# Optimization experiments

Hardware: AMD Instinct MI355X
Metric: run time of the kernel (lower is better)

Reference implementation:

```python
import jax, jax.numpy as jnp
import numpy as np

EMBED_DIM = 512
NUM_HEADS = 16
WIN = (8, 8)
N_TOK = WIN[0] * WIN[1]           # 64 tokens per window
HEAD_DIM = EMBED_DIM // NUM_HEADS  # 32
SCALE = HEAD_DIM ** -0.5
B_WIN = 1024                       # batch * num_windows
NUM_WINDOWS = 256                  # windows per image -> batch images = 4


def _relative_bias_index(window_size):
    wh, ww = window_size
    coords = np.stack(np.meshgrid(np.arange(wh), np.arange(ww), indexing='ij'))  # (2, wh, ww)
    flat = coords.reshape(2, -1)                                   # (2, N)
    rel = (flat[:, :, None] - flat[:, None, :]).transpose(1, 2, 0)  # (N, N, 2)
    rel[:, :, 0] += wh - 1
    rel[:, :, 1] += ww - 1
    rel[:, :, 0] *= 2 * ww - 1
    return rel.sum(-1)  # (N, N) int


def setup_inputs() -> dict:
    key = jax.random.key(0)
    ks = jax.random.split(key, 6)
    x = jax.random.normal(ks[0], (B_WIN, N_TOK, EMBED_DIM), dtype=jnp.float32)
    attention_mask = jax.random.normal(ks[1], (NUM_WINDOWS, N_TOK, N_TOK), dtype=jnp.float32)
    qkv_w = jax.random.normal(ks[2], (EMBED_DIM, 3 * EMBED_DIM), dtype=jnp.float32) * 0.02
    qkv_b = jnp.zeros((3 * EMBED_DIM,), dtype=jnp.float32)
    proj_w = jax.random.normal(ks[3], (EMBED_DIM, EMBED_DIM), dtype=jnp.float32) * 0.02
    proj_b = jnp.zeros((EMBED_DIM,), dtype=jnp.float32)
    n_bias = (2 * WIN[0] - 1) * (2 * WIN[1] - 1)  # 225
    bias_table = jax.random.normal(ks[4], (n_bias, NUM_HEADS), dtype=jnp.float32) * 0.02
    rel_index = jnp.asarray(_relative_bias_index(WIN), dtype=jnp.int32)  # (N, N)
    return {"x": x, "attention_mask": attention_mask, "qkv_w": qkv_w, "qkv_b": qkv_b,
            "proj_w": proj_w, "proj_b": proj_b, "bias_table": bias_table, "rel_index": rel_index}


def reference(x, attention_mask, qkv_w, qkv_b, proj_w, proj_b, bias_table, rel_index):
    B, N, C = x.shape
    nw = attention_mask.shape[0]
    bimg = B // nw
    qkv = x @ qkv_w + qkv_b                              # (B, N, 3C)
    # original rearrange 'b n (h d c) -> d b n h c' groups last dim as (heads, 3, head_dim)
    qkv = qkv.reshape(B, N, NUM_HEADS, 3, HEAD_DIM)
    q, k, v = qkv[..., 0, :], qkv[..., 1, :], qkv[..., 2, :]  # each (B, N, H, hd)
    attn = jnp.einsum('bqhd,bkhd->bhqk', q, k) * SCALE        # (B, H, N, N)
    bias = bias_table[rel_index].transpose(2, 0, 1)           # (H, N, N)
    attn = attn + bias[None]
    attn = attn.reshape(bimg, nw, NUM_HEADS, N, N) + attention_mask[None, :, None]
    attn = jax.nn.softmax(attn, axis=-1).reshape(B, NUM_HEADS, N, N)
    out = jnp.einsum('bhqk,bkhd->bqhd', attn, v).reshape(B, N, C)
    return out @ proj_w + proj_b
```

## Files before the change

### kernel.cpp

```cpp
#include <hip/hip_runtime.h>
#include <hip/hip_bf16.h>


typedef unsigned short u16;
typedef __bf16 bx8 __attribute__((ext_vector_type(8)));
typedef float f4_t __attribute__((ext_vector_type(4)));

#define QKV_ELEMS 33554432ull
#define SCALE 0.17677669529663687f

static __device__ __forceinline__ u16 f2b(float f) {
    return __builtin_bit_cast(u16, (__bf16)f);
}

typedef const unsigned int __attribute__((address_space(1)))* gas_t;
typedef unsigned int __attribute__((address_space(3)))* las_t;
static __device__ __forceinline__ void glds16(const void* g, void* l) {
    __builtin_amdgcn_global_load_lds((gas_t)g, (las_t)l, 16, 0, 0);
}

__global__ void cvt_k(const float* __restrict__ X, u16* __restrict__ Xb) {
    size_t i = ((size_t)blockIdx.x * 256 + threadIdx.x) * 8;
    float4 v0 = *(const float4*)(X + i);
    float4 v1 = *(const float4*)(X + i + 4);
    ushort4 p0, p1;
    p0.x = f2b(v0.x); p0.y = f2b(v0.y); p0.z = f2b(v0.z); p0.w = f2b(v0.w);
    p1.x = f2b(v1.x); p1.y = f2b(v1.y); p1.z = f2b(v1.z); p1.w = f2b(v1.w);
    *(ushort4*)(Xb + i) = p0;
    *(ushort4*)(Xb + i + 4) = p1;
}

__global__ void wt_k(const float* __restrict__ W, u16* __restrict__ Wt,
                     int K, int N) {
    int idx = blockIdx.x * 256 + threadIdx.x;
    if (idx >= N * K) return;
    int n = idx / K, k = idx - n * K;
    Wt[idx] = f2b(W[(size_t)k * N + n]);
}

__global__ void bias_k(const float* __restrict__ bias_table,
                       const int* __restrict__ rel_index,
                       float* __restrict__ bias_full) {
    int idx = blockIdx.x * 256 + threadIdx.x;
    int h = idx >> 12, rc = idx & 4095;
    bias_full[idx] = bias_table[rel_index[rc] * 16 + h];
}

template <int MODE>
__global__ __launch_bounds__(256) void gemm_k(
    const u16* __restrict__ A, const u16* __restrict__ Bt,
    const float* __restrict__ bias, void* __restrict__ Out, int K) {
    const int tid  = threadIdx.x;
    const int wave = tid >> 6, lane = tid & 63;
    const int quad = lane >> 4, l16 = lane & 15;
    const int wm = wave >> 1, wn = wave & 1;
    const int m0 = blockIdx.y * 128, n0 = blockIdx.x * 128;
    const int N = gridDim.x * 128;

    __shared__ alignas(16) u16 a_s[128 * 32];
    __shared__ alignas(16) u16 b_s[128 * 32];

    const int lr = lane >> 2, lc = (lane & 3) * 8;
    const int w16 = wave * 16;

    f4_t acc[4][4];
#pragma unroll
    for (int i = 0; i < 4; ++i)
#pragma unroll
        for (int j = 0; j < 4; ++j) acc[i][j] = (f4_t){0.f, 0.f, 0.f, 0.f};

    for (int kt = 0; kt < K; kt += 32) {
        const u16* Ab = A + (size_t)m0 * K + kt;
        const u16* Bb = Bt + (size_t)n0 * K + kt;
        glds16(Ab + (size_t)(w16 + lr) * K + lc,      &a_s[w16 * 32]);
        glds16(Ab + (size_t)(w16 + 64 + lr) * K + lc, &a_s[(w16 + 64) * 32]);
        glds16(Bb + (size_t)(w16 + lr) * K + lc,      &b_s[w16 * 32]);
        glds16(Bb + (size_t)(w16 + 64 + lr) * K + lc, &b_s[(w16 + 64) * 32]);
        __syncthreads();

        bx8 af[4], bfr[4];
#pragma unroll
        for (int mt = 0; mt < 4; ++mt)
            af[mt] = *(const bx8*)&a_s[(wm * 64 + mt * 16 + l16) * 32 + quad * 8];
#pragma unroll
        for (int nt = 0; nt < 4; ++nt)
            bfr[nt] = *(const bx8*)&b_s[(wn * 64 + nt * 16 + l16) * 32 + quad * 8];
#pragma unroll
        for (int mt = 0; mt < 4; ++mt)
#pragma unroll
            for (int nt = 0; nt < 4; ++nt)
                acc[mt][nt] = __builtin_amdgcn_mfma_f32_16x16x32_bf16(
                    af[mt], bfr[nt], acc[mt][nt], 0, 0, 0);
        __syncthreads();
    }

    if (MODE == 0) {
        u16* qkv = (u16*)Out;
#pragma unroll
        for (int mt = 0; mt < 4; ++mt)
#pragma unroll
            for (int nt = 0; nt < 4; ++nt)
#pragma unroll
                for (int i = 0; i < 4; ++i) {
                    int r = m0 + wm * 64 + mt * 16 + quad * 4 + i;
                    int c = n0 + wn * 64 + nt * 16 + l16;
                    float v = acc[mt][nt][i] + bias[c];
                    int w = r >> 6, tok = r & 63;
                    int h = c / 96, rr = c - h * 96;
                    int which = rr >> 5, dd = rr & 31;
                    qkv[(size_t)which * QKV_ELEMS +
                        ((size_t)((w * 16 + h) * 64 + tok)) * 32 + dd] = f2b(v);
                }
    } else {
        float* Of = (float*)Out;
#pragma unroll
        for (int mt = 0; mt < 4; ++mt)
#pragma unroll
            for (int nt = 0; nt < 4; ++nt)
#pragma unroll
                for (int i = 0; i < 4; ++i) {
                    int r = m0 + wm * 64 + mt * 16 + quad * 4 + i;
                    int c = n0 + wn * 64 + nt * 16 + l16;
                    Of[(size_t)r * N + c] = acc[mt][nt][i] + bias[c];
                }
    }
}

__global__ __launch_bounds__(256) void attn_k(
    const u16* __restrict__ qkv, const float* __restrict__ mask,
    const float* __restrict__ biasf, u16* __restrict__ attn_out) {
    const int bx = blockIdx.x;
    const int w = bx >> 4, h = bx & 15;
    const int wmk = w & 255;
    const int tid = threadIdx.x;
    const int wave = tid >> 6, lane = tid & 63;
    const int quad = lane >> 4, l16 = lane & 15;

    __shared__ alignas(16) u16 q_s[64 * 40];
    __shared__ alignas(16) u16 k_s[64 * 40];
    __shared__ alignas(16) u16 vT[32 * 72];
    __shared__ float s_s[64 * 68];
    __shared__ alignas(16) u16 p_s[64 * 72];

    const size_t base = (size_t)((w << 4) + h) * 2048;
    {
        int tok = tid >> 2, d0 = (tid & 3) * 8;
        uint4 qv = *(const uint4*)(qkv + base + tid * 8);
        *(uint4*)&q_s[tok * 40 + d0] = qv;
        uint4 kv = *(const uint4*)(qkv + QKV_ELEMS + base + tid * 8);
        *(uint4*)&k_s[tok * 40 + d0] = kv;
        uint4 vv = *(const uint4*)(qkv + 2 * QKV_ELEMS + base + tid * 8);
        const u16* pv = (const u16*)&vv;
#pragma unroll
        for (int j = 0; j < 8; ++j) vT[(d0 + j) * 72 + tok] = pv[j];
    }
    __syncthreads();

    {
        bx8 a = *(const bx8*)&q_s[(wave * 16 + l16) * 40 + quad * 8];
#pragma unroll
        for (int nt = 0; nt < 4; ++nt) {
            bx8 b = *(const bx8*)&k_s[(nt * 16 + l16) * 40 + quad * 8];
            f4_t acc = (f4_t){0.f, 0.f, 0.f, 0.f};
            acc = __builtin_amdgcn_mfma_f32_16x16x32_bf16(a, b, acc, 0, 0, 0);
#pragma unroll
            for (int i = 0; i < 4; ++i) {
                int r = wave * 16 + quad * 4 + i;
                int c = nt * 16 + l16;
                float s = acc[i] * SCALE + biasf[(h << 12) + (r << 6) + c] +
                          mask[((size_t)wmk * 64 + r) * 64 + c];
                s_s[r * 68 + c] = s;
            }
        }
    }
    __syncthreads();

    {
        int row = tid >> 2, j = (tid & 3) * 16;
        float mx = -1e30f;
#pragma unroll
        for (int cc = 0; cc < 16; ++cc) mx = fmaxf(mx, s_s[row * 68 + j + cc]);
        mx = fmaxf(mx, __shfl_xor(mx, 1));
        mx = fmaxf(mx, __shfl_xor(mx, 2));
        float e[16], sum = 0.f;
#pragma unroll
        for (int cc = 0; cc < 16; ++cc) {
            e[cc] = __expf(s_s[row * 68 + j + cc] - mx);
            sum += e[cc];
        }
        sum += __shfl_xor(sum, 1);
        sum += __shfl_xor(sum, 2);
        float inv = 1.f / sum;
#pragma unroll
        for (int cc = 0; cc < 16; ++cc) p_s[row * 72 + j + cc] = f2b(e[cc] * inv);
    }
    __syncthreads();

    {
#pragma unroll
        for (int nt = 0; nt < 2; ++nt) {
            f4_t acc = (f4_t){0.f, 0.f, 0.f, 0.f};
#pragma unroll
            for (int ks = 0; ks < 2; ++ks) {
                bx8 a = *(const bx8*)&p_s[(wave * 16 + l16) * 72 + ks * 32 + quad * 8];
                bx8 b = *(const bx8*)&vT[(nt * 16 + l16) * 72 + ks * 32 + quad * 8];
                acc = __builtin_amdgcn_mfma_f32_16x16x32_bf16(a, b, acc, 0, 0, 0);
            }
#pragma unroll
            for (int i = 0; i < 4; ++i) {
                int r = wave * 16 + quad * 4 + i;
                int c = nt * 16 + l16;
                attn_out[((size_t)(w * 64 + r) << 9) + (h << 5) + c] = f2b(acc[i]);
            }
        }
    }
}

extern "C" void kernel_launch(void* const* d_in, const int* in_sizes, int n_in,
                              void* d_out, int out_size, void* d_ws,
                              size_t ws_size, hipStream_t stream) {
    const float* x      = (const float*)d_in[0];
    const float* mask   = (const float*)d_in[1];
    const float* qkv_w  = (const float*)d_in[2];
    const float* qkv_b  = (const float*)d_in[3];
    const float* proj_w = (const float*)d_in[4];
    const float* proj_b = (const float*)d_in[5];
    const float* bias_t = (const float*)d_in[6];
    const int*   rel    = (const int*)d_in[7];
    float* out = (float*)d_out;

    char* ws = (char*)d_ws;
    u16* Wt1 = (u16*)ws;      ws += (size_t)1536 * 512 * 2;
    u16* Wt2 = (u16*)ws;      ws += (size_t)512 * 512 * 2;
    float* biasf = (float*)ws; ws += (size_t)16 * 64 * 64 * 4;
    u16* qkv = (u16*)ws;      ws += 3 * QKV_ELEMS * 2;
    u16* attn = (u16*)ws;     ws += QKV_ELEMS * 2;
    u16* xb = attn;

    cvt_k<<<16384, 256, 0, stream>>>(x, xb);
    wt_k<<<3072, 256, 0, stream>>>(qkv_w, Wt1, 512, 1536);
    wt_k<<<1024, 256, 0, stream>>>(proj_w, Wt2, 512, 512);
    bias_k<<<256, 256, 0, stream>>>(bias_t, rel, biasf);
    gemm_k<0><<<dim3(12, 512), 256, 0, stream>>>(xb, Wt1, qkv_b, qkv, 512);
    attn_k<<<16384, 256, 0, stream>>>(qkv, mask, biasf, attn);
    gemm_k<1><<<dim3(4, 512), 256, 0, stream>>>(attn, Wt2, proj_b, out, 512);
}
```

Measured before the change: 572.1 us.

## Stage GEMM and attention epilogues through LDS for coalesced vector stores

The QKV and projection GEMM epilogues now write accumulators into shared memory first and then issue 16-byte coalesced stores, replacing scattered 2-byte and 4-byte stores. The attention kernel stages its output tile in LDS and writes it in a head-major layout, so the projection GEMM reads its A operand from that blocked layout with contiguous 64-byte rows. The goal is to cut uncoalesced global write traffic, at the cost of extra barriers and LDS round trips in the epilogues.

```diff
diff --git a/kernel.cpp b/kernel.cpp
--- a/kernel.cpp
+++ b/kernel.cpp
@@ -55,10 +55,10 @@
     const int quad = lane >> 4, l16 = lane & 15;
     const int wm = wave >> 1, wn = wave & 1;
     const int m0 = blockIdx.y * 128, n0 = blockIdx.x * 128;
-    const int N = gridDim.x * 128;
-
-    __shared__ alignas(16) u16 a_s[128 * 32];
-    __shared__ alignas(16) u16 b_s[128 * 32];
+
+    __shared__ alignas(16) char smem[17408];
+    u16* a_s = (u16*)smem;
+    u16* b_s = (u16*)(smem + 8192);
 
     const int lr = lane >> 2, lc = (lane & 3) * 8;
     const int w16 = wave * 16;
@@ -70,10 +70,16 @@
         for (int j = 0; j < 4; ++j) acc[i][j] = (f4_t){0.f, 0.f, 0.f, 0.f};
 
     for (int kt = 0; kt < K; kt += 32) {
-        const u16* Ab = A + (size_t)m0 * K + kt;
+        if (MODE == 0) {
+            const u16* Ab = A + (size_t)m0 * K + kt;
+            glds16(Ab + (size_t)(w16 + lr) * K + lc,      &a_s[w16 * 32]);
+            glds16(Ab + (size_t)(w16 + 64 + lr) * K + lc, &a_s[(w16 + 64) * 32]);
+        } else {
+            const u16* Ab = A + (((size_t)(kt >> 5) * 1024 + (m0 >> 6)) << 11);
+            glds16(Ab + ((w16 + lr) << 5) + lc,        &a_s[w16 * 32]);
+            glds16(Ab + 2048 + ((w16 + lr) << 5) + lc, &a_s[(w16 + 64) * 32]);
+        }
         const u16* Bb = Bt + (size_t)n0 * K + kt;
-        glds16(Ab + (size_t)(w16 + lr) * K + lc,      &a_s[w16 * 32]);
-        glds16(Ab + (size_t)(w16 + 64 + lr) * K + lc, &a_s[(w16 + 64) * 32]);
         glds16(Bb + (size_t)(w16 + lr) * K + lc,      &b_s[w16 * 32]);
         glds16(Bb + (size_t)(w16 + 64 + lr) * K + lc, &b_s[(w16 + 64) * 32]);
         __syncthreads();
@@ -94,35 +100,70 @@
         __syncthreads();
     }
 
+    float bv[4];
+#pragma unroll
+    for (int nt = 0; nt < 4; ++nt) bv[nt] = bias[n0 + wn * 64 + nt * 16 + l16];
+
     if (MODE == 0) {
+        u16* c_s = (u16*)smem;
         u16* qkv = (u16*)Out;
-#pragma unroll
-        for (int mt = 0; mt < 4; ++mt)
-#pragma unroll
-            for (int nt = 0; nt < 4; ++nt)
-#pragma unroll
-                for (int i = 0; i < 4; ++i) {
-                    int r = m0 + wm * 64 + mt * 16 + quad * 4 + i;
-                    int c = n0 + wn * 64 + nt * 16 + l16;
-                    float v = acc[mt][nt][i] + bias[c];
-                    int w = r >> 6, tok = r & 63;
-                    int h = c / 96, rr = c - h * 96;
-                    int which = rr >> 5, dd = rr & 31;
-                    qkv[(size_t)which * QKV_ELEMS +
-                        ((size_t)((w * 16 + h) * 64 + tok)) * 32 + dd] = f2b(v);
-                }
+        const int g = tid >> 6, s = tid & 63;
+        const int cgb = n0 + g * 32;
+        const int h = cgb / 96, rr = cgb - h * 96;
+        const int which = rr >> 5;
+#pragma unroll
+        for (int p = 0; p < 2; ++p) {
+            if (wm == p) {
+#pragma unroll
+                for (int mt = 0; mt < 4; ++mt)
+#pragma unroll
+                    for (int nt = 0; nt < 4; ++nt)
+#pragma unroll
+                        for (int i = 0; i < 4; ++i)
+                            c_s[(mt * 16 + quad * 4 + i) * 136 +
+                                wn * 64 + nt * 16 + l16] =
+                                f2b(acc[mt][nt][i] + bv[nt]);
+            }
+            __syncthreads();
+            const int w = (m0 >> 6) + p;
+            u16* dst = qkv + (size_t)which * QKV_ELEMS +
+                       ((size_t)((w << 4) + h) << 11);
+#pragma unroll
+            for (int j = 0; j < 4; ++j) {
+                int idx = s + 64 * j;
+                int tok = idx >> 2, d8 = (idx & 3) * 8;
+                uint4 v = *(const uint4*)&c_s[tok * 136 + g * 32 + d8];
+                *(uint4*)(dst + idx * 8) = v;
+            }
+            __syncthreads();
+        }
     } else {
+        float* c_sf = (float*)smem;
         float* Of = (float*)Out;
 #pragma unroll
-        for (int mt = 0; mt < 4; ++mt)
-#pragma unroll
-            for (int nt = 0; nt < 4; ++nt)
-#pragma unroll
-                for (int i = 0; i < 4; ++i) {
-                    int r = m0 + wm * 64 + mt * 16 + quad * 4 + i;
-                    int c = n0 + wn * 64 + nt * 16 + l16;
-                    Of[(size_t)r * N + c] = acc[mt][nt][i] + bias[c];
-                }
+        for (int p = 0; p < 4; ++p) {
+            if (wm == (p >> 1)) {
+                const int mtb = (p & 1) * 2;
+#pragma unroll
+                for (int mt2 = 0; mt2 < 2; ++mt2)
+#pragma unroll
+                    for (int nt = 0; nt < 4; ++nt)
+#pragma unroll
+                        for (int i = 0; i < 4; ++i)
+                            c_sf[(mt2 * 16 + quad * 4 + i) * 136 +
+                                 wn * 64 + nt * 16 + l16] =
+                                acc[mtb + mt2][nt][i] + bv[nt];
+            }
+            __syncthreads();
+#pragma unroll
+            for (int j = 0; j < 4; ++j) {
+                int fl = tid + 256 * j;
+                int row = fl >> 5, c4 = (fl & 31) * 4;
+                float4 v = *(const float4*)&c_sf[row * 136 + c4];
+                *(float4*)&Of[(size_t)(m0 + p * 32 + row) * 512 + n0 + c4] = v;
+            }
+            __syncthreads();
+        }
     }
 }
 
@@ -139,7 +180,7 @@
     __shared__ alignas(16) u16 q_s[64 * 40];
     __shared__ alignas(16) u16 k_s[64 * 40];
     __shared__ alignas(16) u16 vT[32 * 72];
-    __shared__ float s_s[64 * 68];
+    __shared__ alignas(16) float s_s[64 * 68];
     __shared__ alignas(16) u16 p_s[64 * 72];
 
     const size_t base = (size_t)((w << 4) + h) * 2048;
@@ -197,6 +238,7 @@
     __syncthreads();
 
     {
+        u16* os = (u16*)s_s;
 #pragma unroll
         for (int nt = 0; nt < 2; ++nt) {
             f4_t acc = (f4_t){0.f, 0.f, 0.f, 0.f};
@@ -207,12 +249,14 @@
                 acc = __builtin_amdgcn_mfma_f32_16x16x32_bf16(a, b, acc, 0, 0, 0);
             }
 #pragma unroll
-            for (int i = 0; i < 4; ++i) {
-                int r = wave * 16 + quad * 4 + i;
-                int c = nt * 16 + l16;
-                attn_out[((size_t)(w * 64 + r) << 9) + (h << 5) + c] = f2b(acc[i]);
-            }
-        }
+            for (int i = 0; i < 4; ++i)
+                os[(wave * 16 + quad * 4 + i) * 40 + nt * 16 + l16] =
+                    f2b(acc[i]);
+        }
+        __syncthreads();
+        int tok = tid >> 2, d8 = (tid & 3) * 8;
+        uint4 v = *(const uint4*)&os[tok * 40 + d8];
+        *(uint4*)(attn_out + ((((size_t)h << 10) + w) << 11) + tid * 8) = v;
     }
 }
 
```

After: 542.7 us. 1.05x faster.
